# Kernel optimization log

Hardware: AMD Instinct MI355X
Metric: run time of the kernel (lower is better)

The kernel has to match this reference:

```python
import jax, jax.numpy as jnp
import numpy as np

N_NODES = 100000
N_EDGES = 3200000
D_IN = 16
D_OUT = 32


def setup_inputs() -> dict:
    key = jax.random.key(0)
    ks = jax.random.split(key, 8)
    x = jax.random.normal(ks[0], (N_NODES, D_IN), dtype=jnp.float32)
    edge_index = jax.random.randint(ks[1], (2, N_EDGES), 0, N_NODES, dtype=jnp.int64)
    s = 1.0 / np.sqrt(D_IN)
    # mlp1: Linear(16,16) -> ReLU -> Linear(16,16)
    w1 = jax.random.uniform(ks[2], (D_IN, D_IN), jnp.float32, -s, s)
    b1 = jax.random.uniform(ks[3], (D_IN,), jnp.float32, -s, s)
    w2 = jax.random.uniform(ks[4], (D_IN, D_IN), jnp.float32, -s, s)
    b2 = jax.random.uniform(ks[5], (D_IN,), jnp.float32, -s, s)
    # SAGEConv(16,32): lin_l (neighbors, with bias), lin_r (root, no bias)
    wl = jax.random.uniform(ks[6], (D_IN, D_OUT), jnp.float32, -s, s)
    bl = jnp.zeros((D_OUT,), jnp.float32)
    wr = jax.random.uniform(ks[7], (D_IN, D_OUT), jnp.float32, -s, s)
    return {"x": x, "edge_index": edge_index, "w1": w1, "b1": b1,
            "w2": w2, "b2": b2, "wl": wl, "bl": bl, "wr": wr}


def reference(x, edge_index, w1, b1, w2, b2, wl, bl, wr):
    # MLP: Linear -> ReLU -> Linear
    h = jax.nn.relu(x @ w1 + b1) @ w2 + b2  # [N, 16]
    src, dst = edge_index[0], edge_index[1]
    # mean aggregation of neighbor (source) features at destination nodes
    msg = h[src]  # [E, 16]
    summed = jax.ops.segment_sum(msg, dst, num_segments=N_NODES)  # [N, 16]
    cnt = jax.ops.segment_sum(jnp.ones((msg.shape[0],), h.dtype), dst,
                              num_segments=N_NODES)
    mean = summed / jnp.maximum(cnt, 1.0)[:, None]
    # SAGEConv: lin_l(aggr) + lin_r(root)
    out = mean @ wl + bl + h @ wr  # [N, 32]
    return out
```

## Files before the change

kernel.cpp:

```cpp
#include <hip/hip_runtime.h>

#define D_IN_C 16
#define D_OUT_C 32
#define NB_LOG 6
#define NB (1 << NB_LOG)
#define NB_MASK (NB - 1)
#define MAXBUCK 1600
#define EPB 12800

__global__ __launch_bounds__(256) void mlp_kernel(
    const float* __restrict__ x,
    const float* __restrict__ w1, const float* __restrict__ b1,
    const float* __restrict__ w2, const float* __restrict__ b2,
    float* __restrict__ h, float* __restrict__ summed, int* __restrict__ cnt,
    int* __restrict__ gcount, int nbuck, int n_nodes) {
  __shared__ float sw1[256];
  __shared__ float sw2[256];
  __shared__ float sb1[16];
  __shared__ float sb2[16];
  int t = threadIdx.x;
  sw1[t] = w1[t];
  sw2[t] = w2[t];
  if (t < 16) { sb1[t] = b1[t]; sb2[t] = b2[t]; }
  __syncthreads();

  int n = blockIdx.x * blockDim.x + t;

  if (gcount && n < nbuck) gcount[n] = 0;
  if (n >= n_nodes) return;

  float xi[16];
  const float4* xr = (const float4*)(x + (size_t)n * 16);
  float4 v0 = xr[0], v1 = xr[1], v2 = xr[2], v3 = xr[3];
  xi[0]=v0.x; xi[1]=v0.y; xi[2]=v0.z; xi[3]=v0.w;
  xi[4]=v1.x; xi[5]=v1.y; xi[6]=v1.z; xi[7]=v1.w;
  xi[8]=v2.x; xi[9]=v2.y; xi[10]=v2.z; xi[11]=v2.w;
  xi[12]=v3.x; xi[13]=v3.y; xi[14]=v3.z; xi[15]=v3.w;

  float t1[16];
#pragma unroll
  for (int j = 0; j < 16; ++j) {
    float acc = sb1[j];
#pragma unroll
    for (int k = 0; k < 16; ++k) acc += xi[k] * sw1[k * 16 + j];
    t1[j] = fmaxf(acc, 0.0f);
  }
  float hh[16];
#pragma unroll
  for (int j = 0; j < 16; ++j) {
    float acc = sb2[j];
#pragma unroll
    for (int k = 0; k < 16; ++k) acc += t1[k] * sw2[k * 16 + j];
    hh[j] = acc;
  }

  float4* hw = (float4*)(h + (size_t)n * 16);
  hw[0] = make_float4(hh[0], hh[1], hh[2], hh[3]);
  hw[1] = make_float4(hh[4], hh[5], hh[6], hh[7]);
  hw[2] = make_float4(hh[8], hh[9], hh[10], hh[11]);
  hw[3] = make_float4(hh[12], hh[13], hh[14], hh[15]);

  if (cnt) cnt[n] = 0;
  if (summed) {
    float4* sz = (float4*)(summed + (size_t)n * 16);
    float4 z = make_float4(0.f, 0.f, 0.f, 0.f);
    sz[0] = z; sz[1] = z; sz[2] = z; sz[3] = z;
  }
}

__global__ __launch_bounds__(1024) void hist_kernel(
    const int* __restrict__ dst, int* __restrict__ gcount,
    int nbuck, int n_edges) {
  __shared__ int lcnt[MAXBUCK];
  int t = threadIdx.x;
  for (int i = t; i < MAXBUCK; i += 1024) lcnt[i] = 0;
  __syncthreads();
  int e0 = blockIdx.x * EPB;
  int e1 = e0 + EPB; if (e1 > n_edges) e1 = n_edges;
  for (int e = e0 + t; e < e1; e += 1024)
    atomicAdd(&lcnt[dst[e] >> NB_LOG], 1);
  __syncthreads();
  for (int b = t; b < nbuck; b += 1024) {
    int c = lcnt[b];
    if (c) atomicAdd(&gcount[b], c);
  }
}

__global__ __launch_bounds__(256) void scan_kernel(
    const int* __restrict__ gcount, int* __restrict__ base,
    int* __restrict__ cursor, int nbuck) {
  __shared__ int ps[256];
  int t = threadIdx.x;
  int per = (nbuck + 255) / 256;
  int beg = t * per;
  int end = beg + per; if (end > nbuck) end = nbuck;
  int sum = 0;
  for (int i = beg; i < end; ++i) sum += gcount[i];
  ps[t] = sum;
  __syncthreads();
#pragma unroll
  for (int off = 1; off < 256; off <<= 1) {
    int add = (t >= off) ? ps[t - off] : 0;
    __syncthreads();
    ps[t] += add;
    __syncthreads();
  }
  int run = ps[t] - sum;
  for (int i = beg; i < end; ++i) {
    base[i] = run;
    cursor[i] = run;
    run += gcount[i];
  }
  if (t == 255) base[nbuck] = ps[255];
}

__global__ __launch_bounds__(1024) void bin_kernel(
    const int* __restrict__ src, const int* __restrict__ dst,
    int* __restrict__ cursor, unsigned int* __restrict__ ebuf,
    int nbuck, int n_edges) {
  __shared__ int lcnt[MAXBUCK];
  __shared__ int lspan[MAXBUCK];
  int t = threadIdx.x;
  for (int i = t; i < MAXBUCK; i += 1024) lcnt[i] = 0;
  __syncthreads();
  int e0 = blockIdx.x * EPB;
  int e1 = e0 + EPB; if (e1 > n_edges) e1 = n_edges;
  for (int e = e0 + t; e < e1; e += 1024)
    atomicAdd(&lcnt[dst[e] >> NB_LOG], 1);
  __syncthreads();
  for (int b = t; b < nbuck; b += 1024) {
    int c = lcnt[b];
    lspan[b] = c ? atomicAdd(&cursor[b], c) : 0;
    lcnt[b] = 0;
  }
  __syncthreads();
  for (int e = e0 + t; e < e1; e += 1024) {
    int d = dst[e];
    int b = d >> NB_LOG;
    int r = atomicAdd(&lcnt[b], 1);
    ebuf[lspan[b] + r] =
        ((unsigned int)src[e] << NB_LOG) | (unsigned int)(d & NB_MASK);
  }
}

__global__ __launch_bounds__(256) void agg_out_kernel(
    const float* __restrict__ h, const unsigned int* __restrict__ ebuf,
    const int* __restrict__ base,
    const float* __restrict__ wl, const float* __restrict__ bl,
    const float* __restrict__ wr, float* __restrict__ out, int n_nodes) {
  __shared__ float ssum[NB * 16];
  __shared__ int   scnt[NB];
  __shared__ float swl[512];
  __shared__ float swr[512];
  __shared__ float sbl[32];

  int t = threadIdx.x;
  int b = blockIdx.x;

  for (int i = t; i < 512; i += 256) { swl[i] = wl[i]; swr[i] = wr[i]; }
  if (t < 32) sbl[t] = bl[t];
#pragma unroll
  for (int i = t; i < NB * 16; i += 256) ssum[i] = 0.0f;
  if (t < NB) scnt[t] = 0;
  __syncthreads();

  int beg = base[b];
  int end = base[b + 1];
  int rot = t & 15;

  for (int p = beg + t; p < end; p += 256) {
    unsigned int e2 = ebuf[p];
    int s  = (int)(e2 >> NB_LOG);
    int dl = (int)(e2 & NB_MASK);
    const float* hr = h + (size_t)s * 16;
    float v[16];
#pragma unroll
    for (int j = 0; j < 16; ++j)
      v[j] = hr[(rot + j) & 15];
#pragma unroll
    for (int j = 0; j < 16; ++j)
      atomicAdd(&ssum[dl * 16 + ((rot + j) & 15)], v[j]);
    atomicAdd(&scnt[dl], 1);
  }
  __syncthreads();

  int j = t & 31;
  for (int nl = t >> 5; nl < NB; nl += 8) {
    int n = b * NB + nl;
    if (n >= n_nodes) break;
    float inv = 1.0f / fmaxf((float)scnt[nl], 1.0f);
    float acc = sbl[j];
    const float* hr = h + (size_t)n * 16;
#pragma unroll
    for (int kk = 0; kk < 16; ++kk) {
      float mv = ssum[nl * 16 + kk] * inv;
      acc += mv * swl[kk * 32 + j] + hr[kk] * swr[kk * 32 + j];
    }
    out[(size_t)n * 32 + j] = acc;
  }
}

__global__ __launch_bounds__(256) void scatter_kernel(
    const int* __restrict__ src, const int* __restrict__ dst,
    const float* __restrict__ h, float* __restrict__ summed,
    int* __restrict__ cnt, long long n_edges) {
  long long tid = (long long)blockIdx.x * blockDim.x + threadIdx.x;
  long long e = tid >> 4;
  int k = (int)(tid & 15);
  if (e >= n_edges) return;
  int s = src[e];
  int d = dst[e];
  float val = h[(size_t)s * 16 + k];
  atomicAdd(&summed[(size_t)d * 16 + k], val);
  if (k == 0) atomicAdd(&cnt[d], 1);
}

__global__ __launch_bounds__(256) void out_kernel(
    const float* __restrict__ h, const float* __restrict__ summed,
    const int* __restrict__ cnt,
    const float* __restrict__ wl, const float* __restrict__ bl,
    const float* __restrict__ wr, float* __restrict__ out, int n_nodes) {
  __shared__ float swl[512];
  __shared__ float swr[512];
  __shared__ float sbl[32];
  int t = threadIdx.x;
  for (int i = t; i < 512; i += 256) { swl[i] = wl[i]; swr[i] = wr[i]; }
  if (t < 32) sbl[t] = bl[t];
  __syncthreads();

  int gid = blockIdx.x * 256 + t;
  int n = gid >> 5;
  int j = gid & 31;
  if (n >= n_nodes) return;

  float inv = 1.0f / fmaxf((float)cnt[n], 1.0f);
  const float* hr = h + (size_t)n * 16;
  const float* sr = summed + (size_t)n * 16;
  float acc = sbl[j];
#pragma unroll
  for (int k = 0; k < 16; ++k) {
    acc += sr[k] * inv * swl[k * 32 + j] + hr[k] * swr[k * 32 + j];
  }
  out[(size_t)n * 32 + j] = acc;
}

extern "C" void kernel_launch(void* const* d_in, const int* in_sizes, int n_in,
                              void* d_out, int out_size, void* d_ws, size_t ws_size,
                              hipStream_t stream) {
  const float* x  = (const float*)d_in[0];
  const int* eidx = (const int*)d_in[1];
  const float* w1 = (const float*)d_in[2];
  const float* b1 = (const float*)d_in[3];
  const float* w2 = (const float*)d_in[4];
  const float* b2 = (const float*)d_in[5];
  const float* wl = (const float*)d_in[6];
  const float* bl = (const float*)d_in[7];
  const float* wr = (const float*)d_in[8];
  float* out = (float*)d_out;

  const int n_nodes = in_sizes[0] / D_IN_C;
  const long long n_edges = (long long)in_sizes[1] / 2;
  const int* src = eidx;
  const int* dst = eidx + n_edges;

  const int node_blocks = (n_nodes + 255) / 256;
  const int nbuck = (n_nodes + NB - 1) / NB;
  const int epb_blocks = (int)((n_edges + EPB - 1) / EPB);

  float*        h      = (float*)d_ws;
  int*          gcount = (int*)(h + (size_t)n_nodes * 16);
  int*          cursor = gcount + nbuck;
  int*          base   = cursor + nbuck;
  unsigned int* ebuf   = (unsigned int*)(base + nbuck + 1);

  size_t need = ((size_t)n_nodes * 16 + 3ull * nbuck + 1 + (size_t)n_edges) * 4;

  if (ws_size >= need && nbuck <= MAXBUCK) {
    mlp_kernel<<<node_blocks, 256, 0, stream>>>(
        x, w1, b1, w2, b2, h, nullptr, nullptr, gcount, nbuck, n_nodes);
    hist_kernel<<<epb_blocks, 1024, 0, stream>>>(dst, gcount, nbuck, (int)n_edges);
    scan_kernel<<<1, 256, 0, stream>>>(gcount, base, cursor, nbuck);
    bin_kernel<<<epb_blocks, 1024, 0, stream>>>(src, dst, cursor, ebuf,
                                                nbuck, (int)n_edges);
    agg_out_kernel<<<nbuck, 256, 0, stream>>>(h, ebuf, base, wl, bl, wr, out,
                                              n_nodes);
  } else {
    float* summed = h + (size_t)n_nodes * 16;
    int*   fcnt   = (int*)(summed + (size_t)n_nodes * 16);
    mlp_kernel<<<node_blocks, 256, 0, stream>>>(
        x, w1, b1, w2, b2, h, summed, fcnt, nullptr, 0, n_nodes);
    {
      long long total = n_edges * 16;
      int blocks = (int)((total + 255) / 256);
      scatter_kernel<<<blocks, 256, 0, stream>>>(src, dst, h, summed, fcnt, n_edges);
    }
    {
      long long total = (long long)n_nodes * 32;
      int blocks = (int)((total + 255) / 256);
      out_kernel<<<blocks, 256, 0, stream>>>(h, summed, fcnt, wl, bl, wr, out, n_nodes);
    }
  }
}
```

Baseline: 452.3 us.

## Gather neighbor features with 16 lanes per edge, 8 edges per group

The aggregation loop now assigns each edge to a 16-thread group, one lane per feature. Each group handles 8 consecutive edges and issues all 8 gathers before its LDS atomics. Each h row is read as a coalesced 64-byte access instead of one thread doing 16 strided scalar loads. The cost is that every lane reloads the same edge indices, and the count atomics run on only one lane in sixteen.

Measured after the change: 473.6 us. +4.7%, slower.

```diff
diff --git a/kernel.cpp b/kernel.cpp
--- a/kernel.cpp
+++ b/kernel.cpp
@@ -166,21 +166,51 @@
 
   int beg = base[b];
   int end = base[b + 1];
-  int rot = t & 15;
-
-  for (int p = beg + t; p < end; p += 256) {
-    unsigned int e2 = ebuf[p];
-    int s  = (int)(e2 >> NB_LOG);
-    int dl = (int)(e2 & NB_MASK);
-    const float* hr = h + (size_t)s * 16;
-    float v[16];
-#pragma unroll
-    for (int j = 0; j < 16; ++j)
-      v[j] = hr[(rot + j) & 15];
-#pragma unroll
-    for (int j = 0; j < 16; ++j)
-      atomicAdd(&ssum[dl * 16 + ((rot + j) & 15)], v[j]);
-    atomicAdd(&scnt[dl], 1);
+
+  int g = t >> 4;
+  int k = t & 15;
+
+  for (int p0 = beg + g * 8; p0 < end; p0 += 128) {
+    int m = end - p0; if (m > 8) m = 8;
+    if (m == 8) {
+      unsigned int e0 = ebuf[p0 + 0], e1 = ebuf[p0 + 1];
+      unsigned int e2 = ebuf[p0 + 2], e3 = ebuf[p0 + 3];
+      unsigned int e4 = ebuf[p0 + 4], e5 = ebuf[p0 + 5];
+      unsigned int e6 = ebuf[p0 + 6], e7 = ebuf[p0 + 7];
+      float v0 = h[(size_t)(e0 >> NB_LOG) * 16 + k];
+      float v1 = h[(size_t)(e1 >> NB_LOG) * 16 + k];
+      float v2 = h[(size_t)(e2 >> NB_LOG) * 16 + k];
+      float v3 = h[(size_t)(e3 >> NB_LOG) * 16 + k];
+      float v4 = h[(size_t)(e4 >> NB_LOG) * 16 + k];
+      float v5 = h[(size_t)(e5 >> NB_LOG) * 16 + k];
+      float v6 = h[(size_t)(e6 >> NB_LOG) * 16 + k];
+      float v7 = h[(size_t)(e7 >> NB_LOG) * 16 + k];
+      atomicAdd(&ssum[(e0 & NB_MASK) * 16 + k], v0);
+      atomicAdd(&ssum[(e1 & NB_MASK) * 16 + k], v1);
+      atomicAdd(&ssum[(e2 & NB_MASK) * 16 + k], v2);
+      atomicAdd(&ssum[(e3 & NB_MASK) * 16 + k], v3);
+      atomicAdd(&ssum[(e4 & NB_MASK) * 16 + k], v4);
+      atomicAdd(&ssum[(e5 & NB_MASK) * 16 + k], v5);
+      atomicAdd(&ssum[(e6 & NB_MASK) * 16 + k], v6);
+      atomicAdd(&ssum[(e7 & NB_MASK) * 16 + k], v7);
+      if (k == 0) {
+        atomicAdd(&scnt[e0 & NB_MASK], 1);
+        atomicAdd(&scnt[e1 & NB_MASK], 1);
+        atomicAdd(&scnt[e2 & NB_MASK], 1);
+        atomicAdd(&scnt[e3 & NB_MASK], 1);
+        atomicAdd(&scnt[e4 & NB_MASK], 1);
+        atomicAdd(&scnt[e5 & NB_MASK], 1);
+        atomicAdd(&scnt[e6 & NB_MASK], 1);
+        atomicAdd(&scnt[e7 & NB_MASK], 1);
+      }
+    } else {
+      for (int u = 0; u < m; ++u) {
+        unsigned int ee = ebuf[p0 + u];
+        float v = h[(size_t)(ee >> NB_LOG) * 16 + k];
+        atomicAdd(&ssum[(ee & NB_MASK) * 16 + k], v);
+        if (k == 0) atomicAdd(&scnt[ee & NB_MASK], 1);
+      }
+    }
   }
   __syncthreads();
 
```

## Gather neighbor rows via global_load_lds into per-wave LDS staging buffers

Applied to the files above, without the earlier changes.

Replaces the one-edge-per-thread gather with a wave-cooperative scheme: each 64-lane wave handles 4 edges per step (16 lanes per edge row), issuing 8 batched global_load_lds transfers straight into a per-wave LDS staging area, then doing the LDS atomics from that buffer. The address trick reuses the packed src<<6 encoding as a byte offset (src*64 = row stride). This aims to coalesce the h row reads and raise memory-level parallelism. In exchange it adds a full vmcnt wait per batch and extra LDS, and it relies on the buffer being laid out the way the builtin writes it.

Result: slower. 481.1 us (+6.4%).

```diff
diff --git a/kernel.cpp b/kernel.cpp
--- a/kernel.cpp
+++ b/kernel.cpp
@@ -150,6 +150,7 @@
     const float* __restrict__ wr, float* __restrict__ out, int n_nodes) {
   __shared__ float ssum[NB * 16];
   __shared__ int   scnt[NB];
+  __shared__ float stg[4 * 8 * 64];
   __shared__ float swl[512];
   __shared__ float swr[512];
   __shared__ float sbl[32];
@@ -166,21 +167,41 @@
 
   int beg = base[b];
   int end = base[b + 1];
-  int rot = t & 15;
-
-  for (int p = beg + t; p < end; p += 256) {
-    unsigned int e2 = ebuf[p];
-    int s  = (int)(e2 >> NB_LOG);
-    int dl = (int)(e2 & NB_MASK);
-    const float* hr = h + (size_t)s * 16;
-    float v[16];
-#pragma unroll
-    for (int j = 0; j < 16; ++j)
-      v[j] = hr[(rot + j) & 15];
-#pragma unroll
-    for (int j = 0; j < 16; ++j)
-      atomicAdd(&ssum[dl * 16 + ((rot + j) & 15)], v[j]);
-    atomicAdd(&scnt[dl], 1);
+
+  int wid  = t >> 6;
+  int lane = t & 63;
+  int cl   = lane >> 4;
+  int k    = lane & 15;
+
+  const char* hb = (const char*)h;
+  float* stgw = &stg[wid * 512];
+
+  for (int pb = beg + wid * 32; pb < end; pb += 128) {
+    unsigned int e[8];
+#pragma unroll
+    for (int u = 0; u < 8; ++u) {
+      int idx = pb + 4 * u + cl;
+      int cidx = idx < end ? idx : end - 1;
+      e[u] = ebuf[cidx];
+    }
+#pragma unroll
+    for (int u = 0; u < 8; ++u) {
+      const void* gp = (const void*)(hb + ((e[u] & ~63u) + (unsigned)(k << 2)));
+      __builtin_amdgcn_global_load_lds(
+          (const __attribute__((address_space(1))) void*)gp,
+          (__attribute__((address_space(3))) void*)&stgw[u * 64], 4, 0, 0);
+    }
+    asm volatile("s_waitcnt vmcnt(0)" ::: "memory");
+#pragma unroll
+    for (int u = 0; u < 8; ++u) {
+      int idx = pb + 4 * u + cl;
+      if (idx < end) {
+        float v = stgw[u * 64 + lane];
+        int dl = (int)(e[u] & NB_MASK);
+        atomicAdd(&ssum[dl * 16 + k], v);
+        if (k == 0) atomicAdd(&scnt[dl], 1);
+      }
+    }
   }
   __syncthreads();
 
```

## Split aggregation into two source-range passes with partial sums spilled to output buffer

Applied to the files above, without the earlier changes.

The aggregation kernel now runs twice. Each pass only gathers h rows whose source index falls in one half of the node range, so the gathered working set per pass is smaller and may stay in cache. Partial sums and counts from the first pass are written into each block's slice of the output buffer (the last block uses a workspace area) and reloaded in the second pass. The gather also changes from one edge per thread to 16 threads per edge, one feature each, giving coalesced row loads. In exchange, ebuf is read twice, there is an extra launch and partial results make a round trip through global memory.

Measured after the change: 488.4 us. 1.08x slower.

```diff
diff --git a/kernel.cpp b/kernel.cpp
--- a/kernel.cpp
+++ b/kernel.cpp
@@ -143,11 +143,13 @@
   }
 }
 
-__global__ __launch_bounds__(256) void agg_out_kernel(
+__global__ __launch_bounds__(256) void agg_pass_kernel(
     const float* __restrict__ h, const unsigned int* __restrict__ ebuf,
     const int* __restrict__ base,
     const float* __restrict__ wl, const float* __restrict__ bl,
-    const float* __restrict__ wr, float* __restrict__ out, int n_nodes) {
+    const float* __restrict__ wr, float* __restrict__ out,
+    float* __restrict__ spill_last, int n_nodes,
+    unsigned int lo, unsigned int hi, int final_pass) {
   __shared__ float ssum[NB * 16];
   __shared__ int   scnt[NB];
   __shared__ float swl[512];
@@ -157,32 +159,49 @@
   int t = threadIdx.x;
   int b = blockIdx.x;
 
-  for (int i = t; i < 512; i += 256) { swl[i] = wl[i]; swr[i] = wr[i]; }
-  if (t < 32) sbl[t] = bl[t];
-#pragma unroll
-  for (int i = t; i < NB * 16; i += 256) ssum[i] = 0.0f;
-  if (t < NB) scnt[t] = 0;
+  float* spill = (b == (int)gridDim.x - 1) ? spill_last
+                                           : out + (size_t)b * 2048;
+  int* spillc = (int*)(spill + NB * 16);
+
+  if (final_pass) {
+    for (int i = t; i < 512; i += 256) { swl[i] = wl[i]; swr[i] = wr[i]; }
+    if (t < 32) sbl[t] = bl[t];
+    for (int i = t; i < NB * 16; i += 256) ssum[i] = spill[i];
+    if (t < NB) scnt[t] = spillc[t];
+  } else {
+    for (int i = t; i < NB * 16; i += 256) ssum[i] = 0.0f;
+    if (t < NB) scnt[t] = 0;
+  }
   __syncthreads();
 
   int beg = base[b];
   int end = base[b + 1];
-  int rot = t & 15;
-
-  for (int p = beg + t; p < end; p += 256) {
-    unsigned int e2 = ebuf[p];
-    int s  = (int)(e2 >> NB_LOG);
-    int dl = (int)(e2 & NB_MASK);
-    const float* hr = h + (size_t)s * 16;
-    float v[16];
-#pragma unroll
-    for (int j = 0; j < 16; ++j)
-      v[j] = hr[(rot + j) & 15];
-#pragma unroll
-    for (int j = 0; j < 16; ++j)
-      atomicAdd(&ssum[dl * 16 + ((rot + j) & 15)], v[j]);
-    atomicAdd(&scnt[dl], 1);
-  }
-  __syncthreads();
+
+  int g = t >> 4;
+  int k = t & 15;
+
+  for (int p0 = beg + g * 8; p0 < end; p0 += 128) {
+    int m = end - p0; if (m > 8) m = 8;
+#pragma unroll 8
+    for (int u = 0; u < 8; ++u) {
+      if (u < m) {
+        unsigned int ee = ebuf[p0 + u];
+        unsigned int s = ee >> NB_LOG;
+        if (s >= lo && s < hi) {
+          float v = h[(size_t)s * 16 + k];
+          atomicAdd(&ssum[(ee & NB_MASK) * 16 + k], v);
+          if (k == 0) atomicAdd(&scnt[ee & NB_MASK], 1);
+        }
+      }
+    }
+  }
+  __syncthreads();
+
+  if (!final_pass) {
+    for (int i = t; i < NB * 16; i += 256) spill[i] = ssum[i];
+    if (t < NB) spillc[t] = scnt[t];
+    return;
+  }
 
   int j = t & 31;
   for (int nl = t >> 5; nl < NB; nl += 8) {
@@ -272,8 +291,10 @@
   int*          cursor = gcount + nbuck;
   int*          base   = cursor + nbuck;
   unsigned int* ebuf   = (unsigned int*)(base + nbuck + 1);
-
-  size_t need = ((size_t)n_nodes * 16 + 3ull * nbuck + 1 + (size_t)n_edges) * 4;
+  float*        spill_last = (float*)(ebuf + n_edges);
+
+  size_t need = ((size_t)n_nodes * 16 + 3ull * nbuck + 1 + (size_t)n_edges
+                 + 1088) * 4;
 
   if (ws_size >= need && nbuck <= MAXBUCK) {
     mlp_kernel<<<node_blocks, 256, 0, stream>>>(
@@ -282,8 +303,13 @@
     scan_kernel<<<1, 256, 0, stream>>>(gcount, base, cursor, nbuck);
     bin_kernel<<<epb_blocks, 1024, 0, stream>>>(src, dst, cursor, ebuf,
                                                 nbuck, (int)n_edges);
-    agg_out_kernel<<<nbuck, 256, 0, stream>>>(h, ebuf, base, wl, bl, wr, out,
-                                              n_nodes);
+    unsigned int H = (unsigned int)(n_nodes >> 1);
+    agg_pass_kernel<<<nbuck, 256, 0, stream>>>(
+        h, ebuf, base, wl, bl, wr, out, spill_last, n_nodes,
+        0u, H, 0);
+    agg_pass_kernel<<<nbuck, 256, 0, stream>>>(
+        h, ebuf, base, wl, bl, wr, out, spill_last, n_nodes,
+        H, 0xFFFFFFFFu, 1);
   } else {
     float* summed = h + (size_t)n_nodes * 16;
     int*   fcnt   = (int*)(summed + (size_t)n_nodes * 16);
```
